# Performance work log

Hardware: AMD Instinct MI355X
Metric: run time of the kernel (lower is better)

The kernel has to match this reference:

```python
import jax, jax.numpy as jnp
import numpy as np

EMB = 256

def setup_inputs() -> dict:
    key = jax.random.key(0)
    ks = jax.random.split(key, 7)
    c = EMB
    x = jax.random.normal(ks[0], (4, c, 64, 64), dtype=jnp.float32)
    s = 1.0 / np.sqrt(c)
    Wq = jax.random.uniform(ks[1], (c, c), jnp.float32, -s, s)
    bq = jax.random.uniform(ks[2], (c,), jnp.float32, -s, s)
    Wk = jax.random.uniform(ks[3], (c, c), jnp.float32, -s, s)
    bk = jax.random.uniform(ks[4], (c,), jnp.float32, -s, s)
    Wv = jax.random.uniform(ks[5], (c, c), jnp.float32, -s, s)
    bv = jax.random.uniform(ks[6], (c,), jnp.float32, -s, s)
    return {"x": x, "Wq": Wq, "bq": bq, "Wk": Wk, "bk": bk, "Wv": Wv, "bv": bv}

def reference(x, Wq, bq, Wk, bk, Wv, bv):
    b, c, h, w = x.shape
    scale = jnp.sqrt(jnp.float32(c))
    # [b, n, c] tokens, n = h*w
    xt = x.reshape(b, c, h * w).transpose(0, 2, 1)
    q = jnp.einsum('bnc,dc->bnd', xt, Wq) + bq
    k = jnp.einsum('bnc,dc->bnd', xt, Wk) + bk
    v = jnp.einsum('bnc,dc->bnd', xt, Wv) + bv
    dist = jnp.einsum('bnd,bmd->bnm', q, k) / scale  # [b, n, n]
    dist = jax.nn.softmax(dist, axis=-1)
    mem = jnp.einsum('bnm,bmd->bnd', dist, v)  # [b, n, c]
    # Original: permute(0,1,2) is identity, then raw view(b,c,h,w) -> reshape
    return mem.reshape(b, c, h, w)
```

## Files before the change

### kernel.cpp

```cpp
#include <hip/hip_runtime.h>

typedef __attribute__((ext_vector_type(8))) short short8;
typedef __attribute__((ext_vector_type(4))) short short4_t;
typedef __attribute__((ext_vector_type(4))) float float4_t;
typedef __attribute__((ext_vector_type(16))) float float16_t;

#define NTOK 4096
#define CDIM 256
#define BPB (NTOK * CDIM)
#define C1 0.0901684400555602f

__device__ inline float bf2f(short s) {
    return __uint_as_float(((unsigned)(unsigned short)s) << 16);
}
__device__ inline short f2bf(float f) {
    unsigned u = __float_as_uint(f);
    return (short)((u + 0x7fffu + ((u >> 16) & 1u)) >> 16);
}

__global__ void sniff_dtype(const unsigned* __restrict__ x, int* __restrict__ flag) {
    __shared__ int cnt;
    if (threadIdx.x == 0) cnt = 0;
    __syncthreads();
    int local = 0;
    for (int i = threadIdx.x; i < 1024; i += 256) {
        unsigned e = (x[i] >> 7) & 0xffu;
        if (e >= 100u && e <= 140u) local++;
    }
    atomicAdd(&cnt, local);
    __syncthreads();
    if (threadIdx.x == 0) flag[0] = (cnt >= 512) ? 1 : 0;
}

template <bool PIN>
__global__ __launch_bounds__(256, 1) void qkv4(
    const void* __restrict__ xv,
    const void* __restrict__ Wq, const void* __restrict__ bq,
    const void* __restrict__ Wk, const void* __restrict__ bk,
    const void* __restrict__ Wv, const void* __restrict__ bv,
    const int* __restrict__ flag, int b0,
    short* __restrict__ qbase, short* __restrict__ kbase,
    short* __restrict__ vtbase)
{
    int nt, bl;
    if (PIN) {
        bl = (blockIdx.x >> 1) & 3;
        nt = ((blockIdx.x >> 3) << 1) | (blockIdx.x & 1);
    } else { nt = blockIdx.x; bl = blockIdx.z; }
    const int b = b0 + bl;
    const int n0 = nt * 64;
    const int tid = threadIdx.x;
    const int w = tid >> 6, lane = tid & 63, l15 = lane & 15, qd = lane >> 4;
    const int isbf = flag[0];

    __shared__ short xt[64 * 264];
    __shared__ short wbuf[64 * 256];

    {
        const size_t xb = (size_t)b * CDIM * NTOK + (size_t)tid * NTOK + n0;
        if (isbf) {
            const short* x = (const short*)xv;
            #pragma unroll
            for (int i = 0; i < 8; ++i) {
                short8 v = *(const short8*)(x + xb + i * 8);
                #pragma unroll
                for (int j = 0; j < 8; ++j) xt[(i * 8 + j) * 264 + tid] = v[j];
            }
        } else {
            const float* x = (const float*)xv;
            #pragma unroll
            for (int i = 0; i < 16; ++i) {
                float4 v = *(const float4*)(x + xb + i * 4);
                xt[(i * 4 + 0) * 264 + tid] = f2bf(v.x);
                xt[(i * 4 + 1) * 264 + tid] = f2bf(v.y);
                xt[(i * 4 + 2) * 264 + tid] = f2bf(v.z);
                xt[(i * 4 + 3) * 264 + tid] = f2bf(v.w);
            }
        }
    }
    __syncthreads();

    short8 af[8];
    #pragma unroll
    for (int s = 0; s < 8; ++s)
        af[s] = *(const short8*)&xt[(16 * w + l15) * 264 + s * 32 + qd * 8];

    const void* Ws[3] = { Wq, Wk, Wv };
    const void* bs[3] = { bq, bk, bv };
    short* qdst  = qbase  + (size_t)bl * BPB;
    short* kdst  = kbase  + (size_t)bl * BPB;
    short* vtdst = vtbase + (size_t)bl * BPB;

    float4 wf[16];
    short8 wb8[8];

    #define LOADSLAB(WI, DH)                                                  \
        if (isbf) {                                                           \
            const short* Wp = (const short*)Ws[WI];                           \
            _Pragma("unroll")                                                 \
            for (int u = 0; u < 8; ++u) {                                     \
                const int fb = u * 256 + tid, r = fb >> 5, blk = fb & 31;     \
                wb8[u] = *(const short8*)(Wp + ((DH) * 64 + r) * 256 + blk * 8); \
            }                                                                 \
        } else {                                                              \
            const float* Wp = (const float*)Ws[WI];                           \
            _Pragma("unroll")                                                 \
            for (int u = 0; u < 8; ++u) {                                     \
                const int fb = u * 256 + tid, r = fb >> 5, blk = fb & 31;     \
                wf[2*u]   = *(const float4*)(Wp + ((DH)*64 + r)*256 + blk*8); \
                wf[2*u+1] = *(const float4*)(Wp + ((DH)*64 + r)*256 + blk*8 + 4); \
            }                                                                 \
        }

    LOADSLAB(0, 0);

    for (int sl = 0; sl < 12; ++sl) {
        const int wi = sl >> 2, dh = sl & 3;
        __syncthreads();

        #pragma unroll
        for (int u = 0; u < 8; ++u) {
            const int fb = u * 256 + tid, r = fb >> 5, blk = fb & 31;
            short8 v;
            if (isbf) v = wb8[u];
            else {
                float4 a = wf[2*u], c4 = wf[2*u+1];
                v[0]=f2bf(a.x);  v[1]=f2bf(a.y);  v[2]=f2bf(a.z);  v[3]=f2bf(a.w);
                v[4]=f2bf(c4.x); v[5]=f2bf(c4.y); v[6]=f2bf(c4.z); v[7]=f2bf(c4.w);
            }
            *(short8*)&wbuf[r * 256 + ((blk ^ (r & 31)) * 8)] = v;
        }
        __syncthreads();

        if (sl + 1 < 12) { LOADSLAB((sl + 1) >> 2, (sl + 1) & 3); }

        #pragma unroll
        for (int dt = 0; dt < 4; ++dt) {
            const int rl = dt * 16 + l15;
            float4_t acc = {0.f, 0.f, 0.f, 0.f};
            #pragma unroll
            for (int s = 0; s < 8; ++s) {
                short8 wb = *(const short8*)&wbuf[rl * 256 + (((s * 4 + qd) ^ (rl & 31)) * 8)];
                acc = __builtin_amdgcn_mfma_f32_16x16x32_bf16(af[s], wb, acc, 0, 0, 0);
            }
            const int d = dh * 64 + dt * 16 + l15;
            const float bias = isbf ? bf2f(((const short*)bs[wi])[d])
                                    : ((const float*)bs[wi])[d];
            if (wi < 2) {
                short* dst = (wi == 0) ? qdst : kdst;
                #pragma unroll
                for (int r = 0; r < 4; ++r) {
                    const int n = n0 + 16 * w + 4 * qd + r;
                    dst[(size_t)n * 256 + d] = f2bf(acc[r] + bias);
                }
            } else {
                short4_t pk;
                #pragma unroll
                for (int r = 0; r < 4; ++r) pk[r] = f2bf(acc[r] + bias);
                const int n = n0 + 16 * w + 4 * qd;
                *(short4_t*)(vtdst + (size_t)d * NTOK + n) = pk;
            }
        }
    }
    #undef LOADSLAB
}

template <bool PIN>
__global__ __launch_bounds__(256, 1) void flash9(
    int b0, const short* __restrict__ qb, const short* __restrict__ kb,
    const short* __restrict__ vtb, const int* __restrict__ flag,
    void* __restrict__ outv)
{
    int qt, bl;
    if (PIN) {
        bl = (blockIdx.x >> 1) & 3;
        qt = ((blockIdx.x >> 3) << 1) | (blockIdx.x & 1);
    } else { qt = blockIdx.x; bl = blockIdx.z; }
    const int b = b0 + bl;
    const int q0 = qt * 64;
    const int tid = threadIdx.x;
    const int w = tid >> 6, lane = tid & 63, l31 = lane & 31, h = lane >> 5;
    const int wi = w & 1, wh = w >> 1;

    __shared__ char smem[147456];
    short* kbufA = (short*)smem;
    short* vbufA = (short*)(smem + 65536);
    short* pbufA = (short*)(smem + 131072);

    const short* Q  = qb  + (size_t)bl * BPB;
    const short* K  = kb  + (size_t)bl * BPB;
    const short* VT = vtb + (size_t)bl * BPB;

    short8 qf[16];
    {
        const short* qrow = Q + (size_t)(q0 + 32 * wh + l31) * 256 + h * 8;
        #pragma unroll
        for (int s = 0; s < 16; ++s)
            qf[s] = *(const short8*)(qrow + s * 16);
    }

    float16_t oacc[4];
    #pragma unroll
    for (int dt = 0; dt < 4; ++dt)
        #pragma unroll
        for (int r = 0; r < 16; ++r) oacc[dt][r] = 0.f;
    float lloc = 0.f;

    const int krw = tid >> 5, kgc = tid & 31;
    const int vrw = tid >> 3, vgc = tid & 7;
    const int kread_row = 32 * wi + l31;
    const int prow = 32 * wh + l31;

    short8 kregs[8], vregs[8];
    #pragma unroll
    for (int u = 0; u < 8; ++u) {
        const int r = u * 8 + krw;
        kregs[u] = *(const short8*)(K + (size_t)r * 256 + kgc * 8);
    }
    #pragma unroll
    for (int u = 0; u < 8; ++u) {
        const int r = u * 8 + krw;
        *(short8*)&kbufA[r * 256 + ((kgc ^ (r & 31)) * 8)] = kregs[u];
    }
    #pragma unroll
    for (int u = 0; u < 8; ++u) {
        const int r = u * 8 + krw;
        kregs[u] = *(const short8*)(K + (size_t)(64 + r) * 256 + kgc * 8);
    }
    #pragma unroll
    for (int u = 0; u < 8; ++u) {
        const int r = u * 32 + vrw;
        vregs[u] = *(const short8*)(VT + (size_t)r * NTOK + vgc * 8);
    }
    __syncthreads();

    #pragma unroll 1
    for (int kt = 0; kt < 64; ++kt) {
        short* kcur  = kbufA + (kt & 1) * 16384;
        short* knext = kbufA + ((kt + 1) & 1) * 16384;
        short* vcur  = vbufA + (kt & 1) * 16384;
        short* vprev = vbufA + ((kt + 1) & 1) * 16384;
        short* pcur  = pbufA + (kt & 1) * 4096;
        short* pprev = pbufA + ((kt + 1) & 1) * 4096;

        if (kt < 63) {
            #pragma unroll
            for (int u = 0; u < 8; ++u) {
                const int r = u * 8 + krw;
                *(short8*)&knext[r * 256 + ((kgc ^ (r & 31)) * 8)] = kregs[u];
            }
        }
        #pragma unroll
        for (int u = 0; u < 8; ++u) {
            const int r = u * 32 + vrw;
            *(short8*)&vcur[r * 64 + ((vgc ^ (r & 7)) * 8)] = vregs[u];
        }

        if (kt < 62) {
            const int k2 = (kt + 2) * 64;
            #pragma unroll
            for (int u = 0; u < 8; ++u) {
                const int r = u * 8 + krw;
                kregs[u] = *(const short8*)(K + (size_t)(k2 + r) * 256 + kgc * 8);
            }
        }
        if (kt < 63) {
            const int k1 = (kt + 1) * 64;
            #pragma unroll
            for (int u = 0; u < 8; ++u) {
                const int r = u * 32 + vrw;
                vregs[u] = *(const short8*)(VT + (size_t)r * NTOK + k1 + vgc * 8);
            }
        }

        float16_t se, so;
        #pragma unroll
        for (int r = 0; r < 16; ++r) { se[r] = 0.f; so[r] = 0.f; }
        #pragma unroll
        for (int j = 0; j < 8; ++j) {
            short8 kfa = *(const short8*)
                &kcur[kread_row * 256 + (((4 * j + h) ^ (kread_row & 31)) * 8)];
            se = __builtin_amdgcn_mfma_f32_32x32x16_bf16(kfa, qf[2 * j], se, 0, 0, 0);
            short8 kfb = *(const short8*)
                &kcur[kread_row * 256 + (((4 * j + 2 + h) ^ (kread_row & 31)) * 8)];
            so = __builtin_amdgcn_mfma_f32_32x32x16_bf16(kfb, qf[2 * j + 1], so, 0, 0, 0);
        }

        #pragma unroll
        for (int g2 = 0; g2 < 4; ++g2) {
            short4_t pk;
            #pragma unroll
            for (int r = 0; r < 4; ++r) {
                const float pv = exp2f((se[4 * g2 + r] + so[4 * g2 + r]) * C1);
                lloc += pv;
                pk[r] = f2bf(pv);
            }
            const int gk = 4 * wi + g2;
            *(short4_t*)&pcur[prow * 64 + ((gk ^ (prow & 7)) * 8) + h * 4] = pk;
        }

        if (kt > 0) {
            short8 pa[4];
            #pragma unroll
            for (int s2 = 0; s2 < 4; ++s2)
                pa[s2] = *(const short8*)
                    &pprev[prow * 64 + (((2 * s2 + h) ^ (prow & 7)) * 8)];
            #pragma unroll
            for (int dt = 0; dt < 4; ++dt) {
                const int vr = 128 * wi + 32 * dt + l31;
                #pragma unroll
                for (int s2 = 0; s2 < 4; ++s2) {
                    short8 vf = *(const short8*)
                        &vprev[vr * 64 + (((2 * s2 + h) ^ (vr & 7)) * 8)];
                    oacc[dt] = __builtin_amdgcn_mfma_f32_32x32x16_bf16(pa[s2], vf, oacc[dt], 0, 0, 0);
                }
            }
        }

        __syncthreads();
    }

    {
        short* pprev = pbufA + 4096;
        short* vprev = vbufA + 16384;
        short8 pa[4];
        #pragma unroll
        for (int s2 = 0; s2 < 4; ++s2)
            pa[s2] = *(const short8*)
                &pprev[prow * 64 + (((2 * s2 + h) ^ (prow & 7)) * 8)];
        #pragma unroll
        for (int dt = 0; dt < 4; ++dt) {
            const int vr = 128 * wi + 32 * dt + l31;
            #pragma unroll
            for (int s2 = 0; s2 < 4; ++s2) {
                short8 vf = *(const short8*)
                    &vprev[vr * 64 + (((2 * s2 + h) ^ (vr & 7)) * 8)];
                oacc[dt] = __builtin_amdgcn_mfma_f32_32x32x16_bf16(pa[s2], vf, oacc[dt], 0, 0, 0);
            }
        }
    }

    float* obuf = (float*)smem;
    float* lbuf = (float*)(smem + 66560);

    {
        float v = lloc + __shfl_xor(lloc, 32, 64);
        if (h == 0) lbuf[(32 * wh + l31) * 2 + wi] = v;
    }
    #pragma unroll
    for (int dt = 0; dt < 4; ++dt) {
        const int dim = 128 * wi + 32 * dt + l31;
        #pragma unroll
        for (int r = 0; r < 16; ++r) {
            const int qrow = 32 * wh + (r & 3) + 8 * (r >> 2) + 4 * h;
            obuf[qrow * 260 + dim] = oacc[dt][r];
        }
    }
    __syncthreads();

    {
        const int row = tid >> 2, q4 = (tid & 3) * 64;
        const float inv = 1.0f / (lbuf[2 * row] + lbuf[2 * row + 1]);
        const float* src = obuf + row * 260 + q4;
        const size_t o = (size_t)(b * NTOK + q0 + row) * 256 + q4;
        if (flag[0]) {
            short* op = (short*)outv;
            #pragma unroll
            for (int g = 0; g < 4; ++g) {
                float4 a = *(const float4*)(src + g * 8);
                float4 c4 = *(const float4*)(src + g * 8 + 4);
                short8 pk;
                pk[0]=f2bf(a.x*inv);  pk[1]=f2bf(a.y*inv);
                pk[2]=f2bf(a.z*inv);  pk[3]=f2bf(a.w*inv);
                pk[4]=f2bf(c4.x*inv); pk[5]=f2bf(c4.y*inv);
                pk[6]=f2bf(c4.z*inv); pk[7]=f2bf(c4.w*inv);
                *(short8*)(op + o + g * 8) = pk;
            }
        } else {
            float* op = (float*)outv;
            #pragma unroll
            for (int g = 0; g < 16; ++g) {
                float4 a = *(const float4*)(src + g * 4);
                a.x *= inv; a.y *= inv; a.z *= inv; a.w *= inv;
                *(float4*)(op + o + g * 4) = a;
            }
        }
    }
}

extern "C" void kernel_launch(void* const* d_in, const int* in_sizes, int n_in,
                              void* d_out, int out_size, void* d_ws, size_t ws_size,
                              hipStream_t stream)
{
    const size_t HDR = 256;
    const size_t TB  = (size_t)BPB * 2;
    const size_t avail = ws_size > HDR ? ws_size - HDR : 0;

    int*   flag  = (int*)d_ws;
    short* kbase = (short*)((char*)d_ws + HDR);

    sniff_dtype<<<1, 256, 0, stream>>>((const unsigned*)d_in[0], flag);

    if (avail >= 12 * TB) {
        short* vtbase = kbase  + 4 * (size_t)BPB;
        short* qbase  = vtbase + 4 * (size_t)BPB;
        qkv4<true><<<dim3(256, 1, 1), 256, 0, stream>>>(
            d_in[0], d_in[1], d_in[2], d_in[3], d_in[4], d_in[5], d_in[6],
            flag, 0, qbase, kbase, vtbase);
        flash9<true><<<dim3(256, 1, 1), 256, 0, stream>>>(
            0, qbase, kbase, vtbase, flag, d_out);
        return;
    }

    int nb = 4;
    while (nb > 1 && avail < (size_t)nb * 3 * TB) nb--;
    short* vtbase = kbase + (size_t)nb * BPB;
    short* qbase  = vtbase + (size_t)nb * BPB;

    for (int b0 = 0; b0 < 4; b0 += nb) {
        const int nbc = (4 - b0) < nb ? (4 - b0) : nb;
        qkv4<false><<<dim3(64, 1, nbc), 256, 0, stream>>>(
            d_in[0], d_in[1], d_in[2], d_in[3], d_in[4], d_in[5], d_in[6],
            flag, b0, qbase, kbase, vtbase);
        flash9<false><<<dim3(64, 1, nbc), 256, 0, stream>>>(
            b0, qbase, kbase, vtbase, flag, d_out);
    }
}
```

Before: 257.6 us.

## Split attention over key halves, stream K from registers, async V loads

Weights are pre-converted to bf16 once in a separate kernel, and the QKV projection reads them directly from global memory instead of staging slabs in shared memory. The flash kernel drops the K shared-memory buffer and loads K fragments straight into registers. V tiles are brought in with global_load_lds direct-to-LDS copies, stored with an XOR swizzle that the projection now writes. When enough workspace exists, the key range is split in two across twice as many blocks, and a combine kernel sums the partial outputs and normalisers. Reduced LDS allows two blocks per CU, at the cost of extra partial-output traffic and an additional kernel launch.

New measurement: 334.0 us. 29.7% more time.

```diff
diff --git a/kernel.cpp b/kernel.cpp
--- a/kernel.cpp
+++ b/kernel.cpp
@@ -16,6 +16,11 @@
 __device__ inline short f2bf(float f) {
     unsigned u = __float_as_uint(f);
     return (short)((u + 0x7fffu + ((u >> 16) & 1u)) >> 16);
+}
+__device__ inline void gl_lds16(const void* g, void* l) {
+    __builtin_amdgcn_global_load_lds(
+        (const __attribute__((address_space(1))) unsigned int*)g,
+        (__attribute__((address_space(3))) unsigned int*)l, 16, 0, 0);
 }
 
 __global__ void sniff_dtype(const unsigned* __restrict__ x, int* __restrict__ flag) {
@@ -32,12 +37,32 @@
     if (threadIdx.x == 0) flag[0] = (cnt >= 512) ? 1 : 0;
 }
 
+__global__ __launch_bounds__(256) void wprep(
+    const void* __restrict__ Wq, const void* __restrict__ Wk,
+    const void* __restrict__ Wv, const int* __restrict__ flag,
+    short* __restrict__ Wb)
+{
+    const int base = (blockIdx.x * 256 + threadIdx.x) * 8;
+    const int wsel = base >> 16, off = base & 65535;
+    const void* W = (wsel == 0) ? Wq : (wsel == 1) ? Wk : Wv;
+    short8 v;
+    if (flag[0]) {
+        v = *(const short8*)((const short*)W + off);
+    } else {
+        const float* f = (const float*)W + off;
+        float4 a = *(const float4*)f;
+        float4 c4 = *(const float4*)(f + 4);
+        v[0]=f2bf(a.x);  v[1]=f2bf(a.y);  v[2]=f2bf(a.z);  v[3]=f2bf(a.w);
+        v[4]=f2bf(c4.x); v[5]=f2bf(c4.y); v[6]=f2bf(c4.z); v[7]=f2bf(c4.w);
+    }
+    *(short8*)(Wb + base) = v;
+}
+
 template <bool PIN>
-__global__ __launch_bounds__(256, 1) void qkv4(
-    const void* __restrict__ xv,
-    const void* __restrict__ Wq, const void* __restrict__ bq,
-    const void* __restrict__ Wk, const void* __restrict__ bk,
-    const void* __restrict__ Wv, const void* __restrict__ bv,
+__global__ __launch_bounds__(256, 2) void qkv5(
+    const void* __restrict__ xv, const short* __restrict__ Wb,
+    const void* __restrict__ bq, const void* __restrict__ bk,
+    const void* __restrict__ bv,
     const int* __restrict__ flag, int b0,
     short* __restrict__ qbase, short* __restrict__ kbase,
     short* __restrict__ vtbase)
@@ -54,7 +79,6 @@
     const int isbf = flag[0];
 
     __shared__ short xt[64 * 264];
-    __shared__ short wbuf[64 * 256];
 
     {
         const size_t xb = (size_t)b * CDIM * NTOK + (size_t)tid * NTOK + n0;
@@ -85,111 +109,80 @@
     for (int s = 0; s < 8; ++s)
         af[s] = *(const short8*)&xt[(16 * w + l15) * 264 + s * 32 + qd * 8];
 
-    const void* Ws[3] = { Wq, Wk, Wv };
-    const void* bs[3] = { bq, bk, bv };
     short* qdst  = qbase  + (size_t)bl * BPB;
     short* kdst  = kbase  + (size_t)bl * BPB;
     short* vtdst = vtbase + (size_t)bl * BPB;
 
-    float4 wf[16];
-    short8 wb8[8];
-
-    #define LOADSLAB(WI, DH)                                                  \
-        if (isbf) {                                                           \
-            const short* Wp = (const short*)Ws[WI];                           \
-            _Pragma("unroll")                                                 \
-            for (int u = 0; u < 8; ++u) {                                     \
-                const int fb = u * 256 + tid, r = fb >> 5, blk = fb & 31;     \
-                wb8[u] = *(const short8*)(Wp + ((DH) * 64 + r) * 256 + blk * 8); \
-            }                                                                 \
-        } else {                                                              \
-            const float* Wp = (const float*)Ws[WI];                           \
-            _Pragma("unroll")                                                 \
-            for (int u = 0; u < 8; ++u) {                                     \
-                const int fb = u * 256 + tid, r = fb >> 5, blk = fb & 31;     \
-                wf[2*u]   = *(const float4*)(Wp + ((DH)*64 + r)*256 + blk*8); \
-                wf[2*u+1] = *(const float4*)(Wp + ((DH)*64 + r)*256 + blk*8 + 4); \
-            }                                                                 \
-        }
-
-    LOADSLAB(0, 0);
-
-    for (int sl = 0; sl < 12; ++sl) {
-        const int wi = sl >> 2, dh = sl & 3;
-        __syncthreads();
-
-        #pragma unroll
-        for (int u = 0; u < 8; ++u) {
-            const int fb = u * 256 + tid, r = fb >> 5, blk = fb & 31;
-            short8 v;
-            if (isbf) v = wb8[u];
-            else {
-                float4 a = wf[2*u], c4 = wf[2*u+1];
-                v[0]=f2bf(a.x);  v[1]=f2bf(a.y);  v[2]=f2bf(a.z);  v[3]=f2bf(a.w);
-                v[4]=f2bf(c4.x); v[5]=f2bf(c4.y); v[6]=f2bf(c4.z); v[7]=f2bf(c4.w);
-            }
-            *(short8*)&wbuf[r * 256 + ((blk ^ (r & 31)) * 8)] = v;
-        }
-        __syncthreads();
-
-        if (sl + 1 < 12) { LOADSLAB((sl + 1) >> 2, (sl + 1) & 3); }
-
-        #pragma unroll
-        for (int dt = 0; dt < 4; ++dt) {
-            const int rl = dt * 16 + l15;
-            float4_t acc = {0.f, 0.f, 0.f, 0.f};
-            #pragma unroll
-            for (int s = 0; s < 8; ++s) {
-                short8 wb = *(const short8*)&wbuf[rl * 256 + (((s * 4 + qd) ^ (rl & 31)) * 8)];
-                acc = __builtin_amdgcn_mfma_f32_16x16x32_bf16(af[s], wb, acc, 0, 0, 0);
-            }
-            const int d = dh * 64 + dt * 16 + l15;
-            const float bias = isbf ? bf2f(((const short*)bs[wi])[d])
-                                    : ((const float*)bs[wi])[d];
-            if (wi < 2) {
-                short* dst = (wi == 0) ? qdst : kdst;
+    #pragma unroll 1
+    for (int wsel = 0; wsel < 3; ++wsel) {
+        const short* W = Wb + wsel * 65536;
+        const void* bp = (wsel == 0) ? bq : (wsel == 1) ? bk : bv;
+        #pragma unroll 1
+        for (int dh = 0; dh < 4; ++dh) {
+            #pragma unroll
+            for (int dt = 0; dt < 4; ++dt) {
+                const int d = dh * 64 + dt * 16 + l15;
+                const short* wr = W + (size_t)d * 256 + qd * 8;
+                float4_t acc = {0.f, 0.f, 0.f, 0.f};
                 #pragma unroll
-                for (int r = 0; r < 4; ++r) {
-                    const int n = n0 + 16 * w + 4 * qd + r;
-                    dst[(size_t)n * 256 + d] = f2bf(acc[r] + bias);
+                for (int s = 0; s < 8; ++s) {
+                    short8 wb = *(const short8*)(wr + s * 32);
+                    acc = __builtin_amdgcn_mfma_f32_16x16x32_bf16(af[s], wb, acc, 0, 0, 0);
                 }
-            } else {
-                short4_t pk;
-                #pragma unroll
-                for (int r = 0; r < 4; ++r) pk[r] = f2bf(acc[r] + bias);
-                const int n = n0 + 16 * w + 4 * qd;
-                *(short4_t*)(vtdst + (size_t)d * NTOK + n) = pk;
-            }
-        }
-    }
-    #undef LOADSLAB
-}
-
-template <bool PIN>
-__global__ __launch_bounds__(256, 1) void flash9(
+                const float bias = isbf ? bf2f(((const short*)bp)[d])
+                                        : ((const float*)bp)[d];
+                if (wsel < 2) {
+                    short* dst = (wsel == 0) ? qdst : kdst;
+                    #pragma unroll
+                    for (int r = 0; r < 4; ++r) {
+                        const int n = n0 + 16 * w + 4 * qd + r;
+                        dst[(size_t)n * 256 + d] = f2bf(acc[r] + bias);
+                    }
+                } else {
+                    short4_t pk;
+                    #pragma unroll
+                    for (int r = 0; r < 4; ++r) pk[r] = f2bf(acc[r] + bias);
+                    const int nb4 = 16 * w + 4 * qd;
+                    const int col = (((nb4 >> 3) ^ (d & 7)) << 3) | (nb4 & 7);
+                    *(short4_t*)(vtdst + (size_t)d * NTOK + n0 + col) = pk;
+                }
+            }
+        }
+    }
+}
+
+template <bool PIN, bool SPLIT>
+__global__ __launch_bounds__(256, 2) void flash10(
     int b0, const short* __restrict__ qb, const short* __restrict__ kb,
-    const short* __restrict__ vtb, const int* __restrict__ flag,
-    void* __restrict__ outv)
+    const short* __restrict__ vts, const int* __restrict__ flag,
+    void* __restrict__ outv, float* __restrict__ pO, float* __restrict__ pl)
 {
-    int qt, bl;
-    if (PIN) {
+    int qt, bl, half;
+    if (SPLIT) {
+        bl = (blockIdx.x >> 1) & 3;
+        const int id = ((blockIdx.x >> 3) << 1) | (blockIdx.x & 1);
+        qt = id >> 1; half = id & 1;
+    } else if (PIN) {
         bl = (blockIdx.x >> 1) & 3;
         qt = ((blockIdx.x >> 3) << 1) | (blockIdx.x & 1);
-    } else { qt = blockIdx.x; bl = blockIdx.z; }
+        half = 0;
+    } else { qt = blockIdx.x; bl = blockIdx.z; half = 0; }
+
     const int b = b0 + bl;
     const int q0 = qt * 64;
     const int tid = threadIdx.x;
     const int w = tid >> 6, lane = tid & 63, l31 = lane & 31, h = lane >> 5;
     const int wi = w & 1, wh = w >> 1;
-
-    __shared__ char smem[147456];
-    short* kbufA = (short*)smem;
-    short* vbufA = (short*)(smem + 65536);
-    short* pbufA = (short*)(smem + 131072);
+    const int KT0 = SPLIT ? (half << 5) : 0;
+    const int KT1 = KT0 + (SPLIT ? 32 : 64);
+
+    __shared__ char smem[81920];
+    short* vbufA = (short*)smem;
+    short* pbufA = (short*)(smem + 65536);
 
     const short* Q  = qb  + (size_t)bl * BPB;
     const short* K  = kb  + (size_t)bl * BPB;
-    const short* VT = vtb + (size_t)bl * BPB;
+    const short* VT = vts + (size_t)bl * BPB;
 
     short8 qf[16];
     {
@@ -206,71 +199,33 @@
         for (int r = 0; r < 16; ++r) oacc[dt][r] = 0.f;
     float lloc = 0.f;
 
-    const int krw = tid >> 5, kgc = tid & 31;
-    const int vrw = tid >> 3, vgc = tid & 7;
-    const int kread_row = 32 * wi + l31;
     const int prow = 32 * wh + l31;
-
-    short8 kregs[8], vregs[8];
-    #pragma unroll
-    for (int u = 0; u < 8; ++u) {
-        const int r = u * 8 + krw;
-        kregs[u] = *(const short8*)(K + (size_t)r * 256 + kgc * 8);
-    }
-    #pragma unroll
-    for (int u = 0; u < 8; ++u) {
-        const int r = u * 8 + krw;
-        *(short8*)&kbufA[r * 256 + ((kgc ^ (r & 31)) * 8)] = kregs[u];
-    }
-    #pragma unroll
-    for (int u = 0; u < 8; ++u) {
-        const int r = u * 8 + krw;
-        kregs[u] = *(const short8*)(K + (size_t)(64 + r) * 256 + kgc * 8);
-    }
-    #pragma unroll
-    for (int u = 0; u < 8; ++u) {
-        const int r = u * 32 + vrw;
-        vregs[u] = *(const short8*)(VT + (size_t)r * NTOK + vgc * 8);
-    }
-    __syncthreads();
+    const short* kr0   = K + (size_t)(32 * wi + l31) * 256 + h * 8;
+    const short* vsrc0 = VT + (size_t)(tid >> 3) * NTOK + (tid & 7) * 8;
+
+    short8 kf[16];
+    {
+        const short* kr = kr0 + (size_t)KT0 * 16384;
+        #pragma unroll
+        for (int j = 0; j < 8; ++j) {
+            kf[2 * j]     = *(const short8*)(kr + j * 32);
+            kf[2 * j + 1] = *(const short8*)(kr + j * 32 + 16);
+        }
+    }
 
     #pragma unroll 1
-    for (int kt = 0; kt < 64; ++kt) {
-        short* kcur  = kbufA + (kt & 1) * 16384;
-        short* knext = kbufA + ((kt + 1) & 1) * 16384;
+    for (int kt = KT0; kt < KT1; ++kt) {
         short* vcur  = vbufA + (kt & 1) * 16384;
         short* vprev = vbufA + ((kt + 1) & 1) * 16384;
         short* pcur  = pbufA + (kt & 1) * 4096;
         short* pprev = pbufA + ((kt + 1) & 1) * 4096;
 
-        if (kt < 63) {
-            #pragma unroll
-            for (int u = 0; u < 8; ++u) {
-                const int r = u * 8 + krw;
-                *(short8*)&knext[r * 256 + ((kgc ^ (r & 31)) * 8)] = kregs[u];
-            }
-        }
-        #pragma unroll
-        for (int u = 0; u < 8; ++u) {
-            const int r = u * 32 + vrw;
-            *(short8*)&vcur[r * 64 + ((vgc ^ (r & 7)) * 8)] = vregs[u];
-        }
-
-        if (kt < 62) {
-            const int k2 = (kt + 2) * 64;
-            #pragma unroll
-            for (int u = 0; u < 8; ++u) {
-                const int r = u * 8 + krw;
-                kregs[u] = *(const short8*)(K + (size_t)(k2 + r) * 256 + kgc * 8);
-            }
-        }
-        if (kt < 63) {
-            const int k1 = (kt + 1) * 64;
-            #pragma unroll
-            for (int u = 0; u < 8; ++u) {
-                const int r = u * 32 + vrw;
-                vregs[u] = *(const short8*)(VT + (size_t)r * NTOK + k1 + vgc * 8);
-            }
+        {
+            const short* vs = vsrc0 + kt * 64;
+            short* vd = vcur + tid * 8;
+            #pragma unroll
+            for (int u = 0; u < 8; ++u)
+                gl_lds16(vs + (size_t)u * (32 * NTOK), vd + u * 2048);
         }
 
         float16_t se, so;
@@ -278,12 +233,8 @@
         for (int r = 0; r < 16; ++r) { se[r] = 0.f; so[r] = 0.f; }
         #pragma unroll
         for (int j = 0; j < 8; ++j) {
-            short8 kfa = *(const short8*)
-                &kcur[kread_row * 256 + (((4 * j + h) ^ (kread_row & 31)) * 8)];
-            se = __builtin_amdgcn_mfma_f32_32x32x16_bf16(kfa, qf[2 * j], se, 0, 0, 0);
-            short8 kfb = *(const short8*)
-                &kcur[kread_row * 256 + (((4 * j + 2 + h) ^ (kread_row & 31)) * 8)];
-            so = __builtin_amdgcn_mfma_f32_32x32x16_bf16(kfb, qf[2 * j + 1], so, 0, 0, 0);
+            se = __builtin_amdgcn_mfma_f32_32x32x16_bf16(kf[2 * j],     qf[2 * j],     se, 0, 0, 0);
+            so = __builtin_amdgcn_mfma_f32_32x32x16_bf16(kf[2 * j + 1], qf[2 * j + 1], so, 0, 0, 0);
         }
 
         #pragma unroll
@@ -299,7 +250,7 @@
             *(short4_t*)&pcur[prow * 64 + ((gk ^ (prow & 7)) * 8) + h * 4] = pk;
         }
 
-        if (kt > 0) {
+        if (kt > KT0) {
             short8 pa[4];
             #pragma unroll
             for (int s2 = 0; s2 < 4; ++s2)
@@ -317,6 +268,15 @@
             }
         }
 
+        if (kt + 1 < KT1) {
+            const short* kr = kr0 + (size_t)(kt + 1) * 16384;
+            #pragma unroll
+            for (int j = 0; j < 8; ++j) {
+                kf[2 * j]     = *(const short8*)(kr + j * 32);
+                kf[2 * j + 1] = *(const short8*)(kr + j * 32 + 16);
+            }
+        }
+
         __syncthreads();
     }
 
@@ -339,51 +299,109 @@
             }
         }
     }
-
-    float* obuf = (float*)smem;
-    float* lbuf = (float*)(smem + 66560);
-
-    {
-        float v = lloc + __shfl_xor(lloc, 32, 64);
-        if (h == 0) lbuf[(32 * wh + l31) * 2 + wi] = v;
-    }
-    #pragma unroll
-    for (int dt = 0; dt < 4; ++dt) {
-        const int dim = 128 * wi + 32 * dt + l31;
-        #pragma unroll
-        for (int r = 0; r < 16; ++r) {
-            const int qrow = 32 * wh + (r & 3) + 8 * (r >> 2) + 4 * h;
-            obuf[qrow * 260 + dim] = oacc[dt][r];
-        }
-    }
     __syncthreads();
 
-    {
-        const int row = tid >> 2, q4 = (tid & 3) * 64;
-        const float inv = 1.0f / (lbuf[2 * row] + lbuf[2 * row + 1]);
-        const float* src = obuf + row * 260 + q4;
-        const size_t o = (size_t)(b * NTOK + q0 + row) * 256 + q4;
-        if (flag[0]) {
-            short* op = (short*)outv;
-            #pragma unroll
-            for (int g = 0; g < 4; ++g) {
-                float4 a = *(const float4*)(src + g * 8);
-                float4 c4 = *(const float4*)(src + g * 8 + 4);
-                short8 pk;
-                pk[0]=f2bf(a.x*inv);  pk[1]=f2bf(a.y*inv);
-                pk[2]=f2bf(a.z*inv);  pk[3]=f2bf(a.w*inv);
-                pk[4]=f2bf(c4.x*inv); pk[5]=f2bf(c4.y*inv);
-                pk[6]=f2bf(c4.z*inv); pk[7]=f2bf(c4.w*inv);
-                *(short8*)(op + o + g * 8) = pk;
-            }
-        } else {
-            float* op = (float*)outv;
-            #pragma unroll
-            for (int g = 0; g < 16; ++g) {
-                float4 a = *(const float4*)(src + g * 4);
-                a.x *= inv; a.y *= inv; a.z *= inv; a.w *= inv;
-                *(float4*)(op + o + g * 4) = a;
-            }
+    if (SPLIT) {
+        float* lbuf = (float*)smem;
+        {
+            float v2 = lloc + __shfl_xor(lloc, 32, 64);
+            if (h == 0) lbuf[(32 * wh + l31) * 2 + wi] = v2;
+        }
+        const size_t pidx = (size_t)(bl * 64 + qt) * 2 + half;
+        float* po = pO + pidx * 16384;
+        #pragma unroll
+        for (int dt = 0; dt < 4; ++dt) {
+            const int dim = 128 * wi + 32 * dt + l31;
+            #pragma unroll
+            for (int r = 0; r < 16; ++r) {
+                const int qrow = 32 * wh + (r & 3) + 8 * (r >> 2) + 4 * h;
+                po[qrow * 256 + dim] = oacc[dt][r];
+            }
+        }
+        __syncthreads();
+        if (tid < 64) pl[pidx * 64 + tid] = lbuf[2 * tid] + lbuf[2 * tid + 1];
+    } else {
+        float* obuf = (float*)smem;
+        float* lbuf = (float*)(smem + 66560);
+        {
+            float v2 = lloc + __shfl_xor(lloc, 32, 64);
+            if (h == 0) lbuf[(32 * wh + l31) * 2 + wi] = v2;
+        }
+        #pragma unroll
+        for (int dt = 0; dt < 4; ++dt) {
+            const int dim = 128 * wi + 32 * dt + l31;
+            #pragma unroll
+            for (int r = 0; r < 16; ++r) {
+                const int qrow = 32 * wh + (r & 3) + 8 * (r >> 2) + 4 * h;
+                obuf[qrow * 260 + dim] = oacc[dt][r];
+            }
+        }
+        __syncthreads();
+        {
+            const int row = tid >> 2, q4 = (tid & 3) * 64;
+            const float inv = 1.0f / (lbuf[2 * row] + lbuf[2 * row + 1]);
+            const float* src = obuf + row * 260 + q4;
+            const size_t o = (size_t)(b * NTOK + q0 + row) * 256 + q4;
+            if (flag[0]) {
+                short* op = (short*)outv;
+                #pragma unroll
+                for (int g = 0; g < 4; ++g) {
+                    float4 a  = *(const float4*)(src + g * 8);
+                    float4 c4 = *(const float4*)(src + g * 8 + 4);
+                    short8 pk;
+                    pk[0]=f2bf(a.x*inv);  pk[1]=f2bf(a.y*inv);
+                    pk[2]=f2bf(a.z*inv);  pk[3]=f2bf(a.w*inv);
+                    pk[4]=f2bf(c4.x*inv); pk[5]=f2bf(c4.y*inv);
+                    pk[6]=f2bf(c4.z*inv); pk[7]=f2bf(c4.w*inv);
+                    *(short8*)(op + o + g * 8) = pk;
+                }
+            } else {
+                float* op = (float*)outv;
+                #pragma unroll
+                for (int g = 0; g < 16; ++g) {
+                    float4 a = *(const float4*)(src + g * 4);
+                    a.x *= inv; a.y *= inv; a.z *= inv; a.w *= inv;
+                    *(float4*)(op + o + g * 4) = a;
+                }
+            }
+        }
+    }
+}
+
+__global__ __launch_bounds__(256) void combine(
+    const float* __restrict__ pO, const float* __restrict__ pl,
+    const int* __restrict__ flag, void* __restrict__ outv)
+{
+    const int tile = blockIdx.x, tid = threadIdx.x;
+    const int row = tid >> 2, seg = (tid & 3) * 64;
+    const float* A = pO + (size_t)tile * 32768 + row * 256 + seg;
+    const float* B = A + 16384;
+    const float inv = 1.0f / (pl[tile * 128 + row] + pl[tile * 128 + 64 + row]);
+    const size_t o = ((size_t)tile * 64 + row) * 256 + seg;
+    if (flag[0]) {
+        short* op = (short*)outv;
+        #pragma unroll
+        for (int g = 0; g < 8; ++g) {
+            float4 a  = *(const float4*)(A + g * 8);
+            float4 a2 = *(const float4*)(A + g * 8 + 4);
+            float4 c  = *(const float4*)(B + g * 8);
+            float4 c2 = *(const float4*)(B + g * 8 + 4);
+            short8 pk;
+            pk[0]=f2bf((a.x+c.x)*inv);   pk[1]=f2bf((a.y+c.y)*inv);
+            pk[2]=f2bf((a.z+c.z)*inv);   pk[3]=f2bf((a.w+c.w)*inv);
+            pk[4]=f2bf((a2.x+c2.x)*inv); pk[5]=f2bf((a2.y+c2.y)*inv);
+            pk[6]=f2bf((a2.z+c2.z)*inv); pk[7]=f2bf((a2.w+c2.w)*inv);
+            *(short8*)(op + o + g * 8) = pk;
+        }
+    } else {
+        float* op = (float*)outv;
+        #pragma unroll
+        for (int g = 0; g < 16; ++g) {
+            float4 a = *(const float4*)(A + g * 4);
+            float4 c = *(const float4*)(B + g * 4);
+            a.x = (a.x + c.x) * inv; a.y = (a.y + c.y) * inv;
+            a.z = (a.z + c.z) * inv; a.w = (a.w + c.w) * inv;
+            *(float4*)(op + o + g * 4) = a;
         }
     }
 }
@@ -393,36 +411,50 @@
                               hipStream_t stream)
 {
     const size_t HDR = 256;
+    const size_t WBB = 393216;
     const size_t TB  = (size_t)BPB * 2;
-    const size_t avail = ws_size > HDR ? ws_size - HDR : 0;
-
-    int*   flag  = (int*)d_ws;
-    short* kbase = (short*)((char*)d_ws + HDR);
+    const size_t OFF_K = HDR + WBB;
+    const size_t need_prim  = OFF_K + 12 * TB;
+    const size_t need_split = need_prim + 33554432 + 131072;
+
+    int*   flag = (int*)d_ws;
+    short* Wb   = (short*)((char*)d_ws + HDR);
 
     sniff_dtype<<<1, 256, 0, stream>>>((const unsigned*)d_in[0], flag);
-
-    if (avail >= 12 * TB) {
+    wprep<<<96, 256, 0, stream>>>(d_in[1], d_in[3], d_in[5], flag, Wb);
+
+    if (ws_size >= need_prim) {
+        short* kbase  = (short*)((char*)d_ws + OFF_K);
         short* vtbase = kbase  + 4 * (size_t)BPB;
         short* qbase  = vtbase + 4 * (size_t)BPB;
-        qkv4<true><<<dim3(256, 1, 1), 256, 0, stream>>>(
-            d_in[0], d_in[1], d_in[2], d_in[3], d_in[4], d_in[5], d_in[6],
-            flag, 0, qbase, kbase, vtbase);
-        flash9<true><<<dim3(256, 1, 1), 256, 0, stream>>>(
-            0, qbase, kbase, vtbase, flag, d_out);
+        qkv5<true><<<dim3(256, 1, 1), 256, 0, stream>>>(
+            d_in[0], Wb, d_in[2], d_in[4], d_in[6], flag, 0,
+            qbase, kbase, vtbase);
+        if (ws_size >= need_split) {
+            float* pO = (float*)((char*)d_ws + need_prim);
+            float* pl = (float*)((char*)d_ws + need_prim + 33554432);
+            flash10<true, true><<<dim3(512, 1, 1), 256, 0, stream>>>(
+                0, qbase, kbase, vtbase, flag, d_out, pO, pl);
+            combine<<<dim3(256, 1, 1), 256, 0, stream>>>(pO, pl, flag, d_out);
+        } else {
+            flash10<true, false><<<dim3(256, 1, 1), 256, 0, stream>>>(
+                0, qbase, kbase, vtbase, flag, d_out, nullptr, nullptr);
+        }
         return;
     }
 
     int nb = 4;
-    while (nb > 1 && avail < (size_t)nb * 3 * TB) nb--;
+    while (nb > 1 && ws_size < OFF_K + (size_t)nb * 3 * TB) nb--;
+    short* kbase  = (short*)((char*)d_ws + OFF_K);
     short* vtbase = kbase + (size_t)nb * BPB;
     short* qbase  = vtbase + (size_t)nb * BPB;
 
     for (int b0 = 0; b0 < 4; b0 += nb) {
         const int nbc = (4 - b0) < nb ? (4 - b0) : nb;
-        qkv4<false><<<dim3(64, 1, nbc), 256, 0, stream>>>(
-            d_in[0], d_in[1], d_in[2], d_in[3], d_in[4], d_in[5], d_in[6],
-            flag, b0, qbase, kbase, vtbase);
-        flash9<false><<<dim3(64, 1, nbc), 256, 0, stream>>>(
-            b0, qbase, kbase, vtbase, flag, d_out);
-    }
-}
+        qkv5<false><<<dim3(64, 1, nbc), 256, 0, stream>>>(
+            d_in[0], Wb, d_in[2], d_in[4], d_in[6], flag, b0,
+            qbase, kbase, vtbase);
+        flash10<false, false><<<dim3(64, 1, nbc), 256, 0, stream>>>(
+            b0, qbase, kbase, vtbase, flag, d_out, nullptr, nullptr);
+    }
+}
```
